# Kernel optimization log

Hardware: AMD Instinct MI355X
Metric: run time of the kernel (lower is better)

## Reference

```python
import jax, jax.numpy as jnp
import numpy as np

S = 2048      # seq_len
H = 32        # num_heads
G = 8         # num_groups (KV heads)
D = 128       # head_dim
HPG = H // G  # heads per group
MODEL = H * D


def setup_inputs() -> dict:
    rng = jax.random.key(0)
    ks = jax.random.split(rng, 6)
    return {
        "query": jax.random.normal(ks[0], (S, H, D), jnp.float32),
        "key":   jax.random.normal(ks[1], (S, G, D), jnp.float32),
        "value": jax.random.normal(ks[2], (S, G, D), jnp.float32),
        "mask":  jnp.zeros((S, S), jnp.float32),
        "w_out": jax.random.normal(ks[3], (MODEL, MODEL), jnp.float32) * (MODEL ** -0.5),
        "b_out": jnp.zeros((MODEL,), jnp.float32),
    }


def reference(query, key, value, mask, w_out, b_out):
    # NOTE: the original torch module prepares `mask` but never applies it to
    # the attention scores; we faithfully reproduce that (mask is unused).
    scale = D ** -0.5
    # [S,H,D] -> [H,S,D] -> [G,HPG,S,D]; head h = g*HPG + i (torch .view split)
    q = query.transpose(1, 0, 2).reshape(G, HPG, S, D)
    k = key.transpose(1, 0, 2)    # [G,S,D]
    v = value.transpose(1, 0, 2)  # [G,S,D]
    scores = jnp.einsum('ghqd,gkd->ghqk', q, k) * scale  # [G,HPG,S,S]
    attn = jax.nn.softmax(scores, axis=-1)
    out = jnp.einsum('ghqk,gkd->ghqd', attn, v)          # [G,HPG,S,D]
    # [G,HPG,S,D] -> [H,S,D] -> [S,H,D] -> [S, H*D]
    out = out.reshape(H, S, D).transpose(1, 0, 2).reshape(S, MODEL)
    out = out @ w_out.T + b_out                           # out_proj (Linear)
    return out.reshape(S, H, D)
```

## Files before the change

kernel.cpp:

```cpp
#include <hip/hip_runtime.h>
#include <hip/hip_bf16.h>
#include <stdint.h>

constexpr int S_ = 2048, H_ = 32, G_ = 8, HPG_ = 4, D_ = 128, MODEL_ = 4096;

typedef __attribute__((ext_vector_type(4))) float f32x4;
typedef __attribute__((ext_vector_type(16))) float f32x16;
typedef __attribute__((ext_vector_type(8))) short bf16x8;
typedef __attribute__((ext_vector_type(4))) short bf16x4;

__device__ inline unsigned short f2bf(float f) {
  unsigned u = __float_as_uint(f);
  u += 0x7FFFu + ((u >> 16) & 1u);
  return (unsigned short)(u >> 16);
}

__device__ inline unsigned cvt_pk_bf16(float lo, float hi) {
  unsigned r;
  asm("v_cvt_pk_bf16_f32 %0, %1, %2" : "=v"(r) : "v"(lo), "v"(hi));
  return r;
}

__device__ inline void gload_lds16(const void* g, void* l) {
  __builtin_amdgcn_global_load_lds(
      (const __attribute__((address_space(1))) unsigned int*)g,
      (__attribute__((address_space(3))) unsigned int*)l,
      16, 0, 0);
}

__global__ __launch_bounds__(256) void cvt_f32_to_bf16(
    const float* __restrict__ in, unsigned short* __restrict__ out, int n4) {
  int i = blockIdx.x * 256 + threadIdx.x;
  if (i < n4) {
    float4 v = reinterpret_cast<const float4*>(in)[i];
    bf16x4 o;
    o[0] = f2bf(v.x); o[1] = f2bf(v.y); o[2] = f2bf(v.z); o[3] = f2bf(v.w);
    reinterpret_cast<bf16x4*>(out)[i] = o;
  }
}

__global__ __launch_bounds__(256) void cvt_k_kernel(
    const float* __restrict__ in, unsigned short* __restrict__ out) {
  int i = blockIdx.x * 256 + threadIdx.x;
  int d4 = i & 31, g = (i >> 5) & 7, s = i >> 8;
  float4 v = reinterpret_cast<const float4*>(in)[i];
  bf16x4 o;
  o[0] = f2bf(v.x); o[1] = f2bf(v.y); o[2] = f2bf(v.z); o[3] = f2bf(v.w);
  reinterpret_cast<bf16x4*>(out)[(g * S_ + s) * 32 + d4] = o;
}

__global__ __launch_bounds__(256) void cvt_v_kernel(
    const float* __restrict__ in, unsigned short* __restrict__ out) {
  __shared__ float t[64][33];
  int s0 = blockIdx.x * 64, d0 = blockIdx.y * 32, g = blockIdx.z;
  int tid = threadIdx.x;
#pragma unroll
  for (int p = 0; p < 2; ++p) {
    int idx = p * 256 + tid;
    int s = idx >> 3, dq = (idx & 7) * 4;
    float4 v = *reinterpret_cast<const float4*>(
        in + ((size_t)(s0 + s) * G_ + g) * D_ + d0 + dq);
    t[s][dq] = v.x; t[s][dq + 1] = v.y; t[s][dq + 2] = v.z; t[s][dq + 3] = v.w;
  }
  __syncthreads();
  int d = tid >> 3, sq = (tid & 7) * 8;
  bf16x8 o;
#pragma unroll
  for (int j = 0; j < 8; ++j) o[j] = f2bf(t[sq + j][d]);
  *reinterpret_cast<bf16x8*>(out + ((size_t)g * D_ + d0 + d) * S_ + s0 + sq) = o;
}

constexpr int QB2 = 128, KVB = 32, NT = S_ / KVB;
constexpr float RTHR = 8.0f;

__global__ __launch_bounds__(256, 2) void attn32_kernel(
    const float* __restrict__ q, const unsigned short* __restrict__ kb,
    const unsigned short* __restrict__ vtb, unsigned short* __restrict__ aout) {
  __shared__ __align__(16) char smem[49152];

  const int qt = blockIdx.x, h = blockIdx.y;
  const int g = h >> 2;
  const int tid = threadIdx.x, w = tid >> 6, lane = tid & 63;
  const int l31 = lane & 31, hi = lane >> 5;

  const float scale2 = 0.12751742354783493f;
  bf16x8 qf[8];
  const int qrow = qt * QB2 + w * 32 + l31;
  {
    const float* qp = q + ((size_t)qrow * H_ + h) * D_;
#pragma unroll
    for (int c = 0; c < 8; ++c) {
      const float* p0 = qp + c * 16 + hi * 8;
      float4 a = *(const float4*)p0;
      float4 b = *(const float4*)(p0 + 4);
      bf16x8 f;
      f[0] = f2bf(a.x * scale2); f[1] = f2bf(a.y * scale2);
      f[2] = f2bf(a.z * scale2); f[3] = f2bf(a.w * scale2);
      f[4] = f2bf(b.x * scale2); f[5] = f2bf(b.y * scale2);
      f[6] = f2bf(b.z * scale2); f[7] = f2bf(b.w * scale2);
      qf[c] = f;
    }
  }

  int ks_kv[2], ks_d[2], vs_d[2], vs_kv[2];
#pragma unroll
  for (int hh = 0; hh < 2; ++hh) {
    int p = w * 1024 + hh * 4096 + lane * 16;
    int kvr = p >> 8;
    ks_kv[hh] = kvr;
    ks_d[hh] = ((p & 255) ^ ((kvr & 7) << 4)) >> 1;
    int dr = p >> 6;
    vs_d[hh] = dr;
    vs_kv[hh] = ((p & 63) ^ (((dr >> 1) & 3) << 4)) >> 1;
  }
  const unsigned short* kg = kb + (size_t)g * S_ * D_;
  const unsigned short* vg = vtb + (size_t)g * D_ * S_;

  auto stage = [&](int t, int buf) {
    int kv0 = t * KVB;
    char* Kd = smem + buf * 16384;
    char* Vd = smem + buf * 16384 + 8192;
#pragma unroll
    for (int hh = 0; hh < 2; ++hh) {
      gload_lds16(kg + (size_t)(kv0 + ks_kv[hh]) * D_ + ks_d[hh],
                  Kd + w * 1024 + hh * 4096);
      gload_lds16(vg + (size_t)vs_d[hh] * S_ + kv0 + vs_kv[hh],
                  Vd + w * 1024 + hh * 4096);
    }
  };

  auto qk_mfma = [&](const char* Kd, f32x16& a0, f32x16& a1) {
    __builtin_amdgcn_s_setprio(1);
#pragma unroll
    for (int c = 0; c < 8; ++c) {
      unsigned off = ((unsigned)(l31 * 256 + c * 32 + hi * 16)) ^
                     ((unsigned)(l31 & 7) << 4);
      bf16x8 kf = *(const bf16x8*)(Kd + off);
      if (c & 1)
        a1 = __builtin_amdgcn_mfma_f32_32x32x16_bf16(kf, qf[c], a1, 0, 0, 0);
      else
        a0 = __builtin_amdgcn_mfma_f32_32x32x16_bf16(kf, qf[c], a0, 0, 0, 0);
    }
    __builtin_amdgcn_s_setprio(0);
  };

  f32x16 of[4];
#pragma unroll
  for (int i = 0; i < 4; ++i) of[i] = (f32x16)0.f;
  float m = -1e30f, l = 0.f;

  stage(0, 0);
  stage(1, 1);
  asm volatile("s_waitcnt vmcnt(4)" ::: "memory");
  __builtin_amdgcn_s_barrier();

  f32x16 s0 = (f32x16)0.f, s1 = (f32x16)0.f;
  qk_mfma(smem, s0, s1);

  for (int t = 0; t < NT; ++t) {
    asm volatile("s_waitcnt vmcnt(0)" ::: "memory");
    __builtin_amdgcn_s_barrier();
    if (t + 2 < NT) stage(t + 2, (t + 2) % 3);

    f32x16 sv = s0 + s1;
    if (t + 1 < NT) {
      s0 = (f32x16)0.f; s1 = (f32x16)0.f;
      qk_mfma(smem + ((t + 1) % 3) * 16384, s0, s1);
    }

    float mx8[8];
#pragma unroll
    for (int i = 0; i < 8; ++i) mx8[i] = fmaxf(sv[i], sv[i + 8]);
#pragma unroll
    for (int i = 0; i < 4; ++i) mx8[i] = fmaxf(mx8[i], mx8[i + 4]);
    float tmax = fmaxf(fmaxf(mx8[0], mx8[1]), fmaxf(mx8[2], mx8[3]));
    tmax = fmaxf(tmax, __shfl_xor(tmax, 32));
    if (__any(tmax > m + RTHR)) {
      float mnew = fmaxf(m, tmax);
      float alpha = __builtin_exp2f(m - mnew);
#pragma unroll
      for (int i = 0; i < 4; ++i)
#pragma unroll
        for (int r = 0; r < 16; ++r) of[i][r] *= alpha;
      l *= alpha;
      m = mnew;
    }
    float pv[16], ps[8];
#pragma unroll
    for (int r = 0; r < 16; ++r) pv[r] = __builtin_exp2f(sv[r] - m);
#pragma unroll
    for (int i = 0; i < 8; ++i) ps[i] = pv[i] + pv[i + 8];
#pragma unroll
    for (int i = 0; i < 4; ++i) ps[i] += ps[i + 4];
    float sum = (ps[0] + ps[1]) + (ps[2] + ps[3]);
    sum += __shfl_xor(sum, 32);
    l += sum;

    unsigned pk[8];
#pragma unroll
    for (int b = 0; b < 8; ++b) pk[b] = cvt_pk_bf16(pv[2 * b], pv[2 * b + 1]);
    bf16x8 pf[2];
#pragma unroll
    for (int kc = 0; kc < 2; ++kc) {
      auto sA = __builtin_amdgcn_permlane32_swap(pk[kc * 4 + 0], pk[kc * 4 + 2],
                                                 false, false);
      auto sB = __builtin_amdgcn_permlane32_swap(pk[kc * 4 + 1], pk[kc * 4 + 3],
                                                 false, false);
      unsigned fr[4] = {(unsigned)sA[0], (unsigned)sB[0],
                        (unsigned)sA[1], (unsigned)sB[1]};
      __builtin_memcpy(&pf[kc], fr, 16);
    }

    const char* Vd = smem + (t % 3) * 16384 + 8192;
    __builtin_amdgcn_s_setprio(1);
#pragma unroll
    for (int db = 0; db < 4; ++db) {
      int d = db * 32 + l31;
#pragma unroll
      for (int kc = 0; kc < 2; ++kc) {
        unsigned off = ((unsigned)(d * 64 + kc * 32 + hi * 16)) ^
                       ((unsigned)((d >> 1) & 3) << 4);
        bf16x8 vf = *(const bf16x8*)(Vd + off);
        of[db] = __builtin_amdgcn_mfma_f32_32x32x16_bf16(vf, pf[kc], of[db], 0, 0, 0);
      }
    }
    __builtin_amdgcn_s_setprio(0);
  }

  __syncthreads();
  float inv = 1.0f / l;
  unsigned short* Ol = (unsigned short*)smem;
  const int ql = w * 32 + l31;
#pragma unroll
  for (int db = 0; db < 4; ++db) {
#pragma unroll
    for (int rp = 0; rp < 8; ++rp) {
      int r0 = rp * 2;
      int d0 = db * 32 + (r0 & 3) + 8 * (r0 >> 2) + 4 * hi;
      unsigned pkv = cvt_pk_bf16(of[db][r0] * inv, of[db][r0 + 1] * inv);
      unsigned off = ((unsigned)(ql * 256 + d0 * 2)) ^ ((unsigned)(ql & 7) << 4);
      *(unsigned*)((char*)Ol + off) = pkv;
    }
  }
  __syncthreads();
  const size_t obase = ((size_t)qt * QB2) * MODEL_ + (size_t)h * D_;
#pragma unroll
  for (int pass = 0; pass < 8; ++pass) {
    int row = pass * 16 + (tid >> 4);
    int c = tid & 15;
    unsigned off = ((unsigned)(row * 256 + c * 16)) ^ ((unsigned)(row & 7) << 4);
    bf16x8 vv = *(const bf16x8*)((char*)Ol + off);
    *(bf16x8*)(aout + obase + (size_t)row * MODEL_ + c * 8) = vv;
  }
}

constexpr int BM = 128, BN = 128, BK = 64;

__global__ __launch_bounds__(256, 2) void gemm_bt_bias(
    const unsigned short* __restrict__ A, const unsigned short* __restrict__ B,
    const float* __restrict__ bias, float* __restrict__ C) {
  __shared__ unsigned short As[BM * BK];
  __shared__ unsigned short Bs[BN * BK];

  const int tid = threadIdx.x;
  const int w = tid >> 6, lane = tid & 63;
  const int wr = w >> 1, wc = w & 1;
  const int r16 = lane & 15, g4 = lane >> 4;
  const int row0 = blockIdx.y * BM, col0 = blockIdx.x * BN;

  f32x4 acc[4][4];
#pragma unroll
  for (int m = 0; m < 4; ++m)
#pragma unroll
    for (int n = 0; n < 4; ++n) acc[m][n] = (f32x4)0.f;

  for (int kt = 0; kt < MODEL_ / BK; ++kt) {
    const int k0 = kt * BK;
    __syncthreads();
#pragma unroll
    for (int j = 0; j < 4; ++j) {
      int chunk = w * 4 + j;
      int sb = chunk * 1024 + lane * 16;
      int srow = sb >> 7;
      int lb = sb ^ ((srow & 7) << 4);
      int kk = (lb & 127) >> 1;
      gload_lds16(A + (size_t)(row0 + srow) * MODEL_ + k0 + kk,
                  (char*)As + chunk * 1024);
      gload_lds16(B + (size_t)(col0 + srow) * MODEL_ + k0 + kk,
                  (char*)Bs + chunk * 1024);
    }
    asm volatile("s_waitcnt vmcnt(0)" ::: "memory");
    __syncthreads();

#pragma unroll
    for (int kc = 0; kc < 2; ++kc) {
      bf16x8 af[4], bfr[4];
#pragma unroll
      for (int m = 0; m < 4; ++m) {
        int row = wr * 64 + m * 16 + r16;
        unsigned off = ((unsigned)(row * 128 + (kc * 32 + g4 * 8) * 2)) ^ ((row & 7) << 4);
        af[m] = *(bf16x8*)((char*)As + off);
      }
#pragma unroll
      for (int n = 0; n < 4; ++n) {
        int row = wc * 64 + n * 16 + r16;
        unsigned off = ((unsigned)(row * 128 + (kc * 32 + g4 * 8) * 2)) ^ ((row & 7) << 4);
        bfr[n] = *(bf16x8*)((char*)Bs + off);
      }
#pragma unroll
      for (int m = 0; m < 4; ++m)
#pragma unroll
        for (int n = 0; n < 4; ++n)
          acc[m][n] = __builtin_amdgcn_mfma_f32_16x16x32_bf16(af[m], bfr[n], acc[m][n], 0, 0, 0);
    }
  }

#pragma unroll
  for (int n = 0; n < 4; ++n) {
    int col = col0 + wc * 64 + n * 16 + r16;
    float bv = bias[col];
#pragma unroll
    for (int m = 0; m < 4; ++m) {
      int rbase = row0 + wr * 64 + m * 16 + g4 * 4;
#pragma unroll
      for (int j = 0; j < 4; ++j)
        C[(size_t)(rbase + j) * MODEL_ + col] = acc[m][n][j] + bv;
    }
  }
}

extern "C" void kernel_launch(void* const* d_in, const int* in_sizes, int n_in,
                              void* d_out, int out_size, void* d_ws, size_t ws_size,
                              hipStream_t stream) {
  const float* q = (const float*)d_in[0];
  const float* k = (const float*)d_in[1];
  const float* v = (const float*)d_in[2];
  const float* w_out = (const float*)d_in[4];
  const float* b_out = (const float*)d_in[5];
  float* out = (float*)d_out;

  unsigned short* attn_bf = (unsigned short*)d_ws;
  unsigned short* xreg = attn_bf + (size_t)S_ * MODEL_;
  unsigned short* k_bf = xreg;
  unsigned short* vt_bf = xreg + (size_t)G_ * S_ * D_;
  unsigned short* w_bf = xreg;
  if (ws_size < ((size_t)S_ * MODEL_ + (size_t)MODEL_ * MODEL_) * 2) return;

  cvt_k_kernel<<<S_ * G_ * D_ / 4 / 256, 256, 0, stream>>>(k, k_bf);
  dim3 vg(S_ / 64, D_ / 32, G_);
  cvt_v_kernel<<<vg, 256, 0, stream>>>(v, vt_bf);

  dim3 ag(S_ / QB2, H_);
  attn32_kernel<<<ag, 256, 0, stream>>>(q, k_bf, vt_bf, attn_bf);

  cvt_f32_to_bf16<<<(MODEL_ * MODEL_ / 4) / 256, 256, 0, stream>>>(
      w_out, w_bf, MODEL_ * MODEL_ / 4);

  dim3 gg(MODEL_ / BN, S_ / BM);
  gemm_bt_bias<<<gg, 256, 0, stream>>>(attn_bf, w_bf, b_out, out);
}
```

Before: 194.9 us.

## Switch attention K/V pipeline to four LDS buffers with barrier every two tiles

Replaces the triple-buffered K/V staging, which synchronised every KV tile, with a four-slot ring in 64 KB of LDS. Two tiles are now staged per step, and the waitcnt plus barrier runs once per pair of tiles. The aim is to halve barrier and wait overhead and give loads more slack. In exchange it drops the software pipelining that overlapped the next tile's QK MFMAs with the current tile's softmax, so QK, softmax and PV now run back-to-back within each tile, and LDS use per block grows.

```diff
diff --git a/kernel.cpp b/kernel.cpp
--- a/kernel.cpp
+++ b/kernel.cpp
@@ -76,7 +76,7 @@
 __global__ __launch_bounds__(256, 2) void attn32_kernel(
     const float* __restrict__ q, const unsigned short* __restrict__ kb,
     const unsigned short* __restrict__ vtb, unsigned short* __restrict__ aout) {
-  __shared__ __align__(16) char smem[49152];
+  __shared__ __align__(16) char smem[65536];
 
   const int qt = blockIdx.x, h = blockIdx.y;
   const int g = h >> 2;
@@ -116,10 +116,10 @@
   const unsigned short* kg = kb + (size_t)g * S_ * D_;
   const unsigned short* vg = vtb + (size_t)g * D_ * S_;
 
-  auto stage = [&](int t, int buf) {
+  auto stage = [&](int t) {
     int kv0 = t * KVB;
-    char* Kd = smem + buf * 16384;
-    char* Vd = smem + buf * 16384 + 8192;
+    char* Kd = smem + (t & 3) * 16384;
+    char* Vd = Kd + 8192;
 #pragma unroll
     for (int hh = 0; hh < 2; ++hh) {
       gload_lds16(kg + (size_t)(kv0 + ks_kv[hh]) * D_ + ks_d[hh],
@@ -129,7 +129,16 @@
     }
   };
 
-  auto qk_mfma = [&](const char* Kd, f32x16& a0, f32x16& a1) {
+  f32x16 of[4];
+#pragma unroll
+  for (int i = 0; i < 4; ++i) of[i] = (f32x16)0.f;
+  float m = -1e30f, l = 0.f;
+
+  auto process = [&](int t) {
+    const char* Kd = smem + (t & 3) * 16384;
+    const char* Vd = Kd + 8192;
+
+    f32x16 s0 = (f32x16)0.f, s1 = (f32x16)0.f;
     __builtin_amdgcn_s_setprio(1);
 #pragma unroll
     for (int c = 0; c < 8; ++c) {
@@ -137,36 +146,12 @@
                      ((unsigned)(l31 & 7) << 4);
       bf16x8 kf = *(const bf16x8*)(Kd + off);
       if (c & 1)
-        a1 = __builtin_amdgcn_mfma_f32_32x32x16_bf16(kf, qf[c], a1, 0, 0, 0);
+        s1 = __builtin_amdgcn_mfma_f32_32x32x16_bf16(kf, qf[c], s1, 0, 0, 0);
       else
-        a0 = __builtin_amdgcn_mfma_f32_32x32x16_bf16(kf, qf[c], a0, 0, 0, 0);
+        s0 = __builtin_amdgcn_mfma_f32_32x32x16_bf16(kf, qf[c], s0, 0, 0, 0);
     }
     __builtin_amdgcn_s_setprio(0);
-  };
-
-  f32x16 of[4];
-#pragma unroll
-  for (int i = 0; i < 4; ++i) of[i] = (f32x16)0.f;
-  float m = -1e30f, l = 0.f;
-
-  stage(0, 0);
-  stage(1, 1);
-  asm volatile("s_waitcnt vmcnt(4)" ::: "memory");
-  __builtin_amdgcn_s_barrier();
-
-  f32x16 s0 = (f32x16)0.f, s1 = (f32x16)0.f;
-  qk_mfma(smem, s0, s1);
-
-  for (int t = 0; t < NT; ++t) {
-    asm volatile("s_waitcnt vmcnt(0)" ::: "memory");
-    __builtin_amdgcn_s_barrier();
-    if (t + 2 < NT) stage(t + 2, (t + 2) % 3);
-
     f32x16 sv = s0 + s1;
-    if (t + 1 < NT) {
-      s0 = (f32x16)0.f; s1 = (f32x16)0.f;
-      qk_mfma(smem + ((t + 1) % 3) * 16384, s0, s1);
-    }
 
     float mx8[8];
 #pragma unroll
@@ -211,7 +196,6 @@
       __builtin_memcpy(&pf[kc], fr, 16);
     }
 
-    const char* Vd = smem + (t % 3) * 16384 + 8192;
     __builtin_amdgcn_s_setprio(1);
 #pragma unroll
     for (int db = 0; db < 4; ++db) {
@@ -225,6 +209,19 @@
       }
     }
     __builtin_amdgcn_s_setprio(0);
+  };
+
+  stage(0); stage(1);
+  asm volatile("s_waitcnt vmcnt(0)" ::: "memory");
+  __builtin_amdgcn_s_barrier();
+  stage(2); stage(3);
+
+  for (int t = 0; t < NT; t += 2) {
+    process(t);
+    process(t + 1);
+    asm volatile("s_waitcnt vmcnt(0)" ::: "memory");
+    __builtin_amdgcn_s_barrier();
+    if (t + 4 < NT) { stage(t + 4); stage(t + 5); }
   }
 
   __syncthreads();
```

Result: faster. 190.5 us (-2.3%).
